# Kernel optimization log

Hardware: AMD Instinct MI355X
Metric: run time of the kernel (lower is better)

Reference implementation:

```python
import jax, jax.numpy as jnp
import numpy as np

B, C, H, W = 16, 512, 32, 32
HEADS = 8
GROUPS = 32
EPS = 1e-5


def setup_inputs() -> dict:
    key = jax.random.key(0)
    ks = jax.random.split(key, 6)
    x = jax.random.normal(ks[0], (B, C, H, W), dtype=jnp.float32)
    gn_scale = jnp.ones((C,), dtype=jnp.float32)
    gn_bias = jnp.zeros((C,), dtype=jnp.float32)
    # 1x1 convs stored as dense matrices [out, in]
    qkv_w = jax.random.normal(ks[1], (3 * C, C), dtype=jnp.float32) * (1.0 / np.sqrt(C))
    proj_w = jax.random.normal(ks[2], (C, C), dtype=jnp.float32) * (1.0 / np.sqrt(C))
    proj_b = jax.random.normal(ks[3], (C,), dtype=jnp.float32) * 0.01
    return {"x": x, "gn_scale": gn_scale, "gn_bias": gn_bias,
            "qkv_w": qkv_w, "proj_w": proj_w, "proj_b": proj_b}


def _forward(x, gn_scale, gn_bias, qkv_w, proj_w, proj_b):
    b, c, h, w = x.shape
    d = c // HEADS  # head dim
    n = h * w
    # GroupNorm over (channels_per_group, h, w)
    xg = x.reshape(b, GROUPS, c // GROUPS, h, w)
    mu = jnp.mean(xg, axis=(2, 3, 4), keepdims=True)
    var = jnp.var(xg, axis=(2, 3, 4), keepdims=True)
    xn = ((xg - mu) * jax.lax.rsqrt(var + EPS)).reshape(b, c, h, w)
    xn = xn * gn_scale[None, :, None, None] + gn_bias[None, :, None, None]
    # 1x1 conv QKV: [b, 3c, n]
    qkv = jnp.einsum('oc,bcn->bon', qkv_w, xn.reshape(b, c, n))
    # split order: (qkv, heads, d)
    qkv = qkv.reshape(b, 3, HEADS, d, n)
    q, k, v = qkv[:, 0], qkv[:, 1], qkv[:, 2]  # each [b, heads, d, n]
    k = jax.nn.softmax(k, axis=-1)
    att = jnp.einsum('bhdn,bhen->bhde', k, v)          # [b, heads, d, d]
    out = jnp.einsum('bhde,bhdn->bhen', att, q)        # [b, heads, d, n]
    out = out.reshape(b, c, h, w)
    # 1x1 proj conv with bias
    out = jnp.einsum('oc,bchw->bohw', proj_w, out) + proj_b[None, :, None, None]
    return out


def reference(x, gn_scale, gn_bias, qkv_w, proj_w, proj_b):
    return _forward(x, gn_scale, gn_bias, qkv_w, proj_w, proj_b)
```

## Files before the change

### kernel.cpp

```cpp
#include <hip/hip_runtime.h>
#include <cstdint>
#include <cstddef>

#define B_ 16
#define C_ 512
#define N_ 1024
#define HEADS_ 8
#define D_ 64
#define CPG_ 16

typedef __bf16 bf16;
typedef bf16 bf16x4 __attribute__((ext_vector_type(4)));
typedef bf16 bf16x8 __attribute__((ext_vector_type(8)));
typedef bf16 bf16x16 __attribute__((ext_vector_type(16)));
typedef float f32x4 __attribute__((ext_vector_type(4)));

__device__ __forceinline__ void gload16(void* lds, const void* g) {
    __builtin_amdgcn_global_load_lds(
        (__attribute__((address_space(1))) void*)(void*)g,
        (__attribute__((address_space(3))) void*)lds, 16, 0, 0);
}

__global__ __launch_bounds__(256) void f32_to_bf16_k(const float* __restrict__ s,
                                                     bf16* __restrict__ d, int n) {
    int i = (blockIdx.x * 256 + threadIdx.x) * 4;
    if (i < n) {
        f32x4 v = *(const f32x4*)(s + i);
        bf16x4 o = {(bf16)v[0], (bf16)v[1], (bf16)v[2], (bf16)v[3]};
        *(bf16x4*)(d + i) = o;
    }
}

__global__ __launch_bounds__(256) void gn_kernel(const float* __restrict__ x,
                                                 const float* __restrict__ gamma,
                                                 const float* __restrict__ beta,
                                                 bf16* __restrict__ xnT) {
    const int blk = blockIdx.x;
    const int b = blk >> 5, g = blk & 31;
    const int c0 = g * CPG_;
    const float* xb = x + ((size_t)b * C_ + c0) * N_;
    const int t = threadIdx.x;

    f32x4 vals[CPG_];
    float sum = 0.f, ssq = 0.f;
#pragma unroll
    for (int c = 0; c < CPG_; ++c) {
        f32x4 v = *(const f32x4*)(xb + c * N_ + t * 4);
        vals[c] = v;
#pragma unroll
        for (int j = 0; j < 4; ++j) { sum += v[j]; ssq += v[j] * v[j]; }
    }
#pragma unroll
    for (int off = 32; off >= 1; off >>= 1) {
        sum += __shfl_xor(sum, off);
        ssq += __shfl_xor(ssq, off);
    }
    __shared__ float red[2][4];
    const int wv = t >> 6, lane = t & 63;
    if (lane == 0) { red[0][wv] = sum; red[1][wv] = ssq; }
    __syncthreads();
    sum = red[0][0] + red[0][1] + red[0][2] + red[0][3];
    ssq = red[1][0] + red[1][1] + red[1][2] + red[1][3];
    const float inv = 1.f / (float)(CPG_ * N_);
    float mean = sum * inv;
    float var = ssq * inv - mean * mean;
    float rstd = rsqrtf(var + 1e-5f);
    float ga[CPG_], be[CPG_];
#pragma unroll
    for (int c = 0; c < CPG_; ++c) {
        float gm = gamma[c0 + c] * rstd;
        ga[c] = gm;
        be[c] = beta[c0 + c] - mean * gm;
    }
#pragma unroll
    for (int j = 0; j < 4; ++j) {
        int n = t * 4 + j;
        bf16x16 o;
#pragma unroll
        for (int c = 0; c < CPG_; ++c) o[c] = (bf16)(vals[c][j] * ga[c] + be[c]);
        *(bf16x16*)(xnT + ((size_t)b * N_ + n) * C_ + c0) = o;
    }
}

template <int EPI>
__global__ __launch_bounds__(256, 2) void gemm_bt(const bf16* __restrict__ A,
                                                  const bf16* __restrict__ Bt,
                                                  int M, int N, int K,
                                                  void* __restrict__ o0,
                                                  void* __restrict__ o1,
                                                  void* __restrict__ o2,
                                                  const float* __restrict__ bias) {
    __shared__ __align__(16) bf16 As[2][128][64];
    __shared__ __align__(16) bf16 Bs[2][128][64];
    const int t = threadIdx.x;
    const int lane = t & 63, wv = t >> 6;
    const int wr = wv >> 1, wc = wv & 1;
    const int bn = blockIdx.x, bm = blockIdx.y, b = blockIdx.z;
    const bf16* Ab = A + (size_t)bm * 128 * K;
    const bf16* Bb = Bt + ((size_t)b * N + (size_t)bn * 128) * K;

    f32x4 acc[4][4];
#pragma unroll
    for (int mi = 0; mi < 4; ++mi)
#pragma unroll
        for (int ni = 0; ni < 4; ++ni) acc[mi][ni] = f32x4{0.f, 0.f, 0.f, 0.f};

    const int nk = K >> 6;

    auto stage = [&](int buf, int kt) {
#pragma unroll
        for (int rnd = 0; rnd < 4; ++rnd) {
            int idx = rnd * 256 + t;
            int row = idx >> 3, pb = idx & 7;
            int srcb = pb ^ (row & 7);
            gload16((char*)&As[buf][0][0] + (size_t)idx * 16,
                    Ab + (size_t)row * K + kt * 64 + srcb * 8);
        }
#pragma unroll
        for (int rnd = 0; rnd < 4; ++rnd) {
            int idx = rnd * 256 + t;
            int row = idx >> 3, pb = idx & 7;
            int srcb = pb ^ (row & 7);
            gload16((char*)&Bs[buf][0][0] + (size_t)idx * 16,
                    Bb + (size_t)row * K + kt * 64 + srcb * 8);
        }
    };
    auto compute = [&](int buf) {
#pragma unroll
        for (int ks = 0; ks < 2; ++ks) {
            bf16x8 af[4], bfr[4];
#pragma unroll
            for (int mi = 0; mi < 4; ++mi) {
                int r = wr * 64 + mi * 16 + (lane & 15);
                int bi = (ks * 4 + (lane >> 4)) ^ (r & 7);
                af[mi] = *(const bf16x8*)&As[buf][r][bi * 8];
            }
#pragma unroll
            for (int ni = 0; ni < 4; ++ni) {
                int r = wc * 64 + ni * 16 + (lane & 15);
                int bi = (ks * 4 + (lane >> 4)) ^ (r & 7);
                bfr[ni] = *(const bf16x8*)&Bs[buf][r][bi * 8];
            }
#pragma unroll
            for (int mi = 0; mi < 4; ++mi)
#pragma unroll
                for (int ni = 0; ni < 4; ++ni)
                    acc[mi][ni] = __builtin_amdgcn_mfma_f32_16x16x32_bf16(
                        af[mi], bfr[ni], acc[mi][ni], 0, 0, 0);
        }
    };

    stage(0, 0);
    for (int kt = 0; kt < nk; ++kt) {
        const int cur = kt & 1;
        if (kt + 1 < nk) {
            stage(cur ^ 1, kt + 1);
            asm volatile("s_waitcnt vmcnt(8)" ::: "memory");
        } else {
            asm volatile("s_waitcnt vmcnt(0)" ::: "memory");
        }
        __builtin_amdgcn_s_barrier();
        __builtin_amdgcn_sched_barrier(0);
        compute(cur);
        __builtin_amdgcn_s_barrier();
    }

    const int rowb = bm * 128 + wr * 64;
    const int colb = bn * 128 + wc * 64;
#pragma unroll
    for (int mi = 0; mi < 4; ++mi) {
#pragma unroll
        for (int ni = 0; ni < 4; ++ni) {
            int r0 = rowb + mi * 16 + (lane >> 4) * 4;
            int cc = colb + ni * 16 + (lane & 15);
            if constexpr (EPI == 0) {
                bf16* qT = (bf16*)o0;
                bf16* klog = (bf16*)o1;
                bf16* vb = (bf16*)o2;
                if (r0 < 512) {
                    int h = r0 >> 6, d = r0 & 63;
                    bf16x4 pk;
#pragma unroll
                    for (int j = 0; j < 4; ++j) pk[j] = (bf16)acc[mi][ni][j];
                    *(bf16x4*)(qT + (((size_t)b * HEADS_ + h) * N_ + cc) * D_ + d) = pk;
                } else {
                    bf16* dst = (r0 < 1024) ? klog : vb;
                    int h = (r0 >> 6) & 7, d = r0 & 63;
                    bf16* p = dst + (((size_t)b * HEADS_ + h) * D_ + d) * N_ + cc;
#pragma unroll
                    for (int j = 0; j < 4; ++j) p[(size_t)j * N_] = (bf16)acc[mi][ni][j];
                }
            } else {
                float* outp = (float*)o0;
#pragma unroll
                for (int j = 0; j < 4; ++j)
                    outp[((size_t)b * C_ + r0 + j) * N_ + cc] = acc[mi][ni][j] + bias[r0 + j];
            }
        }
    }
}

__global__ __launch_bounds__(256) void softmax_k(const bf16* __restrict__ klog,
                                                 bf16* __restrict__ ksm) {
    const int row = blockIdx.x * 4 + (threadIdx.x >> 6);
    const int lane = threadIdx.x & 63;
    const bf16* rp = klog + (size_t)row * N_;
    float v[16];
    float mx = -1e30f;
#pragma unroll
    for (int i = 0; i < 2; ++i) {
        bf16x8 u = *(const bf16x8*)(rp + ((size_t)lane + 64 * i) * 8);
#pragma unroll
        for (int j = 0; j < 8; ++j) {
            v[i * 8 + j] = (float)u[j];
            mx = fmaxf(mx, v[i * 8 + j]);
        }
    }
#pragma unroll
    for (int off = 32; off >= 1; off >>= 1) mx = fmaxf(mx, __shfl_xor(mx, off));
    float s = 0.f;
#pragma unroll
    for (int i = 0; i < 16; ++i) { v[i] = __expf(v[i] - mx); s += v[i]; }
#pragma unroll
    for (int off = 32; off >= 1; off >>= 1) s += __shfl_xor(s, off);
    float inv = 1.f / s;
    bf16* op = ksm + (size_t)row * N_;
#pragma unroll
    for (int i = 0; i < 2; ++i) {
        bf16x8 o;
#pragma unroll
        for (int j = 0; j < 8; ++j) o[j] = (bf16)(v[i * 8 + j] * inv);
        *(bf16x8*)(op + ((size_t)lane + 64 * i) * 8) = o;
    }
}

__global__ __launch_bounds__(256) void attn1_kernel(const bf16* __restrict__ ksm,
                                                    const bf16* __restrict__ vb,
                                                    float* __restrict__ attP) {
    __shared__ float attp[2][64][64];
    const int blk = blockIdx.x;
    const int bh = blk >> 1, half = blk & 1;
    const int t = threadIdx.x, lane = t & 63, wv = t >> 6;
    const bf16* kb = ksm + (size_t)bh * D_ * N_;
    const bf16* vv = vb + (size_t)bh * D_ * N_;

    f32x4 acc[4][4];
#pragma unroll
    for (int mi = 0; mi < 4; ++mi)
#pragma unroll
        for (int ni = 0; ni < 4; ++ni) acc[mi][ni] = f32x4{0.f, 0.f, 0.f, 0.f};

    const int k0 = half * 512 + wv * 128;
#pragma unroll
    for (int kk = 0; kk < 128; kk += 32) {
        bf16x8 af[4], bfr[4];
#pragma unroll
        for (int mi = 0; mi < 4; ++mi)
            af[mi] = *(const bf16x8*)(kb + (size_t)(mi * 16 + (lane & 15)) * N_ + k0 + kk + (lane >> 4) * 8);
#pragma unroll
        for (int ni = 0; ni < 4; ++ni)
            bfr[ni] = *(const bf16x8*)(vv + (size_t)(ni * 16 + (lane & 15)) * N_ + k0 + kk + (lane >> 4) * 8);
#pragma unroll
        for (int mi = 0; mi < 4; ++mi)
#pragma unroll
            for (int ni = 0; ni < 4; ++ni)
                acc[mi][ni] = __builtin_amdgcn_mfma_f32_16x16x32_bf16(
                    af[mi], bfr[ni], acc[mi][ni], 0, 0, 0);
    }
    if (wv < 2) {
#pragma unroll
        for (int mi = 0; mi < 4; ++mi)
#pragma unroll
            for (int ni = 0; ni < 4; ++ni)
#pragma unroll
                for (int j = 0; j < 4; ++j)
                    attp[wv][mi * 16 + (lane >> 4) * 4 + j][ni * 16 + (lane & 15)] = acc[mi][ni][j];
    }
    __syncthreads();
    if (wv >= 2) {
#pragma unroll
        for (int mi = 0; mi < 4; ++mi)
#pragma unroll
            for (int ni = 0; ni < 4; ++ni)
#pragma unroll
                for (int j = 0; j < 4; ++j)
                    attp[wv - 2][mi * 16 + (lane >> 4) * 4 + j][ni * 16 + (lane & 15)] += acc[mi][ni][j];
    }
    __syncthreads();
    float* op = attP + (size_t)blk * 4096;
    for (int i = t; i < 4096; i += 256) {
        int d = i >> 6, e = i & 63;
        op[i] = attp[0][d][e] + attp[1][d][e];
    }
}

__global__ __launch_bounds__(256) void attn2_kernel(const float* __restrict__ attP,
                                                    const bf16* __restrict__ qT,
                                                    bf16* __restrict__ o2T) {
    __shared__ __align__(16) bf16 attT[64][64];
    const int blk = blockIdx.x;
    const int bh = blk >> 2, nc = blk & 3;
    const int b = bh >> 3, h = bh & 7;
    const int t = threadIdx.x, lane = t & 63, wv = t >> 6;
    const float* p0 = attP + (size_t)(bh * 2) * 4096;
    const float* p1 = p0 + 4096;
    for (int i = t; i < 4096; i += 256) {
        int d = i >> 6, e = i & 63;
        attT[e][d ^ ((e & 7) << 3)] = (bf16)(p0[i] + p1[i]);
    }
    __syncthreads();

    const bf16* qb = qT + (size_t)bh * N_ * D_;
    const int n0 = nc * 256 + wv * 64;
    f32x4 a2[4][4];
#pragma unroll
    for (int mi = 0; mi < 4; ++mi)
#pragma unroll
        for (int ni = 0; ni < 4; ++ni) a2[mi][ni] = f32x4{0.f, 0.f, 0.f, 0.f};
#pragma unroll
    for (int ks = 0; ks < 2; ++ks) {
        bf16x8 af[4], bfr[4];
#pragma unroll
        for (int mi = 0; mi < 4; ++mi) {
            int r = mi * 16 + (lane & 15);
            int cb = ks * 32 + (lane >> 4) * 8;
            af[mi] = *(const bf16x8*)&attT[r][cb ^ ((r & 7) << 3)];
        }
#pragma unroll
        for (int ni = 0; ni < 4; ++ni)
            bfr[ni] = *(const bf16x8*)(qb + (size_t)(n0 + ni * 16 + (lane & 15)) * D_ + ks * 32 + (lane >> 4) * 8);
#pragma unroll
        for (int mi = 0; mi < 4; ++mi)
#pragma unroll
            for (int ni = 0; ni < 4; ++ni)
                a2[mi][ni] = __builtin_amdgcn_mfma_f32_16x16x32_bf16(
                    af[mi], bfr[ni], a2[mi][ni], 0, 0, 0);
    }
#pragma unroll
    for (int mi = 0; mi < 4; ++mi) {
#pragma unroll
        for (int ni = 0; ni < 4; ++ni) {
            int e0 = mi * 16 + (lane >> 4) * 4;
            int nn = n0 + ni * 16 + (lane & 15);
            bf16x4 pk;
#pragma unroll
            for (int j = 0; j < 4; ++j) pk[j] = (bf16)a2[mi][ni][j];
            *(bf16x4*)(o2T + ((size_t)b * N_ + nn) * C_ + h * D_ + e0) = pk;
        }
    }
}

extern "C" void kernel_launch(void* const* d_in, const int* in_sizes, int n_in,
                              void* d_out, int out_size, void* d_ws, size_t ws_size,
                              hipStream_t stream) {
    const float* x = (const float*)d_in[0];
    const float* gn_scale = (const float*)d_in[1];
    const float* gn_bias = (const float*)d_in[2];
    const float* qkv_w = (const float*)d_in[3];
    const float* proj_w = (const float*)d_in[4];
    const float* proj_b = (const float*)d_in[5];
    float* out = (float*)d_out;

    const size_t elems = (size_t)B_ * C_ * N_;
    const size_t plane = (size_t)B_ * HEADS_ * D_ * N_;
    char* w = (char*)d_ws;
    bf16* xnT = (bf16*)w;   w += elems * 2;
    bf16* qT = (bf16*)w;    w += plane * 2;
    bf16* klog = (bf16*)w;  w += plane * 2;
    bf16* ksm = (bf16*)w;   w += plane * 2;
    bf16* vbuf = (bf16*)w;  w += plane * 2;
    float* attP = (float*)w; w += (size_t)256 * 4096 * 4;
    bf16* wqkv = (bf16*)w;  w += (size_t)3 * C_ * C_ * 2;
    bf16* wproj = (bf16*)w; w += (size_t)C_ * C_ * 2;
    bf16* o2T = xnT;

    f32_to_bf16_k<<<768, 256, 0, stream>>>(qkv_w, wqkv, 3 * C_ * C_);
    f32_to_bf16_k<<<256, 256, 0, stream>>>(proj_w, wproj, C_ * C_);
    gn_kernel<<<512, 256, 0, stream>>>(x, gn_scale, gn_bias, xnT);
    gemm_bt<0><<<dim3(8, 12, 16), 256, 0, stream>>>(wqkv, xnT, 1536, 1024, 512,
                                                    (void*)qT, (void*)klog, (void*)vbuf, nullptr);
    softmax_k<<<2048, 256, 0, stream>>>(klog, ksm);
    attn1_kernel<<<256, 256, 0, stream>>>(ksm, vbuf, attP);
    attn2_kernel<<<512, 256, 0, stream>>>(attP, qT, o2T);
    gemm_bt<1><<<dim3(8, 4, 16), 256, 0, stream>>>(wproj, o2T, 512, 1024, 512,
                                                   (void*)out, nullptr, nullptr, proj_b);
}
```

Before: 181.6 us.

## Fuse softmax normalization into attn1 via row stats; merge weight conversions

The softmax kernel now writes only per-row max and reciprocal sum instead of a full normalized K tensor. attn1 reads the raw K logits and applies exp and scale on the fly while loading operands. This removes one bf16 plane write and read, about 16 MB. The two weight-conversion launches are merged into one, and the templated GEMM is split into two specialized kernels with compile-time K. In exchange, attn1 does more exp work in its inner loop.

```diff
diff --git a/kernel.cpp b/kernel.cpp
--- a/kernel.cpp
+++ b/kernel.cpp
@@ -8,6 +8,7 @@
 #define HEADS_ 8
 #define D_ 64
 #define CPG_ 16
+#define KDIM 512
 
 typedef __bf16 bf16;
 typedef bf16 bf16x4 __attribute__((ext_vector_type(4)));
@@ -21,14 +22,19 @@
         (__attribute__((address_space(3))) void*)lds, 16, 0, 0);
 }
 
-__global__ __launch_bounds__(256) void f32_to_bf16_k(const float* __restrict__ s,
-                                                     bf16* __restrict__ d, int n) {
-    int i = (blockIdx.x * 256 + threadIdx.x) * 4;
-    if (i < n) {
-        f32x4 v = *(const f32x4*)(s + i);
-        bf16x4 o = {(bf16)v[0], (bf16)v[1], (bf16)v[2], (bf16)v[3]};
-        *(bf16x4*)(d + i) = o;
-    }
+__global__ __launch_bounds__(256) void convert_w(const float* __restrict__ qkv_w,
+                                                 const float* __restrict__ proj_w,
+                                                 bf16* __restrict__ wqkv,
+                                                 bf16* __restrict__ wproj) {
+    const int bid = blockIdx.x;
+    const float* s;
+    bf16* d;
+    int i;
+    if (bid < 768) { s = qkv_w; d = wqkv; i = bid * 1024 + threadIdx.x * 4; }
+    else           { s = proj_w; d = wproj; i = (bid - 768) * 1024 + threadIdx.x * 4; }
+    f32x4 v = *(const f32x4*)(s + i);
+    bf16x4 o = {(bf16)v[0], (bf16)v[1], (bf16)v[2], (bf16)v[3]};
+    *(bf16x4*)(d + i) = o;
 }
 
 __global__ __launch_bounds__(256) void gn_kernel(const float* __restrict__ x,
@@ -82,22 +88,19 @@
     }
 }
 
-template <int EPI>
-__global__ __launch_bounds__(256, 2) void gemm_bt(const bf16* __restrict__ A,
-                                                  const bf16* __restrict__ Bt,
-                                                  int M, int N, int K,
-                                                  void* __restrict__ o0,
-                                                  void* __restrict__ o1,
-                                                  void* __restrict__ o2,
-                                                  const float* __restrict__ bias) {
+__global__ __launch_bounds__(256, 2) void qkv_gemm(const bf16* __restrict__ A,
+                                                   const bf16* __restrict__ Bt,
+                                                   bf16* __restrict__ qT,
+                                                   bf16* __restrict__ klog,
+                                                   bf16* __restrict__ vb) {
     __shared__ __align__(16) bf16 As[2][128][64];
     __shared__ __align__(16) bf16 Bs[2][128][64];
     const int t = threadIdx.x;
     const int lane = t & 63, wv = t >> 6;
     const int wr = wv >> 1, wc = wv & 1;
     const int bn = blockIdx.x, bm = blockIdx.y, b = blockIdx.z;
-    const bf16* Ab = A + (size_t)bm * 128 * K;
-    const bf16* Bb = Bt + ((size_t)b * N + (size_t)bn * 128) * K;
+    const bf16* Ab = A + (size_t)bm * 128 * KDIM;
+    const bf16* Bb = Bt + ((size_t)b * N_ + (size_t)bn * 128) * KDIM;
 
     f32x4 acc[4][4];
 #pragma unroll
@@ -105,7 +108,7 @@
 #pragma unroll
         for (int ni = 0; ni < 4; ++ni) acc[mi][ni] = f32x4{0.f, 0.f, 0.f, 0.f};
 
-    const int nk = K >> 6;
+    const int nk = KDIM >> 6;
 
     auto stage = [&](int buf, int kt) {
 #pragma unroll
@@ -114,7 +117,7 @@
             int row = idx >> 3, pb = idx & 7;
             int srcb = pb ^ (row & 7);
             gload16((char*)&As[buf][0][0] + (size_t)idx * 16,
-                    Ab + (size_t)row * K + kt * 64 + srcb * 8);
+                    Ab + (size_t)row * KDIM + kt * 64 + srcb * 8);
         }
 #pragma unroll
         for (int rnd = 0; rnd < 4; ++rnd) {
@@ -122,7 +125,7 @@
             int row = idx >> 3, pb = idx & 7;
             int srcb = pb ^ (row & 7);
             gload16((char*)&Bs[buf][0][0] + (size_t)idx * 16,
-                    Bb + (size_t)row * K + kt * 64 + srcb * 8);
+                    Bb + (size_t)row * KDIM + kt * 64 + srcb * 8);
         }
     };
     auto compute = [&](int buf) {
@@ -173,35 +176,119 @@
         for (int ni = 0; ni < 4; ++ni) {
             int r0 = rowb + mi * 16 + (lane >> 4) * 4;
             int cc = colb + ni * 16 + (lane & 15);
-            if constexpr (EPI == 0) {
-                bf16* qT = (bf16*)o0;
-                bf16* klog = (bf16*)o1;
-                bf16* vb = (bf16*)o2;
-                if (r0 < 512) {
-                    int h = r0 >> 6, d = r0 & 63;
-                    bf16x4 pk;
-#pragma unroll
-                    for (int j = 0; j < 4; ++j) pk[j] = (bf16)acc[mi][ni][j];
-                    *(bf16x4*)(qT + (((size_t)b * HEADS_ + h) * N_ + cc) * D_ + d) = pk;
-                } else {
-                    bf16* dst = (r0 < 1024) ? klog : vb;
-                    int h = (r0 >> 6) & 7, d = r0 & 63;
-                    bf16* p = dst + (((size_t)b * HEADS_ + h) * D_ + d) * N_ + cc;
-#pragma unroll
-                    for (int j = 0; j < 4; ++j) p[(size_t)j * N_] = (bf16)acc[mi][ni][j];
-                }
+            if (r0 < 512) {
+                int h = r0 >> 6, d = r0 & 63;
+                bf16x4 pk;
+#pragma unroll
+                for (int j = 0; j < 4; ++j) pk[j] = (bf16)acc[mi][ni][j];
+                *(bf16x4*)(qT + (((size_t)b * HEADS_ + h) * N_ + cc) * D_ + d) = pk;
             } else {
-                float* outp = (float*)o0;
-#pragma unroll
-                for (int j = 0; j < 4; ++j)
-                    outp[((size_t)b * C_ + r0 + j) * N_ + cc] = acc[mi][ni][j] + bias[r0 + j];
+                bf16* dst = (r0 < 1024) ? klog : vb;
+                int h = (r0 >> 6) & 7, d = r0 & 63;
+                bf16* p = dst + (((size_t)b * HEADS_ + h) * D_ + d) * N_ + cc;
+#pragma unroll
+                for (int j = 0; j < 4; ++j) p[(size_t)j * N_] = (bf16)acc[mi][ni][j];
             }
         }
     }
 }
 
-__global__ __launch_bounds__(256) void softmax_k(const bf16* __restrict__ klog,
-                                                 bf16* __restrict__ ksm) {
+__global__ __launch_bounds__(256, 2) void proj_gemm(const bf16* __restrict__ A,
+                                                    const bf16* __restrict__ Bt,
+                                                    float* __restrict__ outp,
+                                                    const float* __restrict__ bias) {
+    __shared__ __align__(16) bf16 As[2][128][64];
+    __shared__ __align__(16) bf16 Bs[2][128][64];
+    const int t = threadIdx.x;
+    const int lane = t & 63, wv = t >> 6;
+    const int wr = wv >> 1, wc = wv & 1;
+    const int bn = blockIdx.x, bm = blockIdx.y, b = blockIdx.z;
+    const bf16* Ab = A + (size_t)bm * 128 * KDIM;
+    const bf16* Bb = Bt + ((size_t)b * N_ + (size_t)bn * 128) * KDIM;
+
+    f32x4 acc[4][4];
+#pragma unroll
+    for (int mi = 0; mi < 4; ++mi)
+#pragma unroll
+        for (int ni = 0; ni < 4; ++ni) acc[mi][ni] = f32x4{0.f, 0.f, 0.f, 0.f};
+
+    const int nk = KDIM >> 6;
+
+    auto stage = [&](int buf, int kt) {
+#pragma unroll
+        for (int rnd = 0; rnd < 4; ++rnd) {
+            int idx = rnd * 256 + t;
+            int row = idx >> 3, pb = idx & 7;
+            int srcb = pb ^ (row & 7);
+            gload16((char*)&As[buf][0][0] + (size_t)idx * 16,
+                    Ab + (size_t)row * KDIM + kt * 64 + srcb * 8);
+        }
+#pragma unroll
+        for (int rnd = 0; rnd < 4; ++rnd) {
+            int idx = rnd * 256 + t;
+            int row = idx >> 3, pb = idx & 7;
+            int srcb = pb ^ (row & 7);
+            gload16((char*)&Bs[buf][0][0] + (size_t)idx * 16,
+                    Bb + (size_t)row * KDIM + kt * 64 + srcb * 8);
+        }
+    };
+    auto compute = [&](int buf) {
+#pragma unroll
+        for (int ks = 0; ks < 2; ++ks) {
+            bf16x8 af[4], bfr[4];
+#pragma unroll
+            for (int mi = 0; mi < 4; ++mi) {
+                int r = wr * 64 + mi * 16 + (lane & 15);
+                int bi = (ks * 4 + (lane >> 4)) ^ (r & 7);
+                af[mi] = *(const bf16x8*)&As[buf][r][bi * 8];
+            }
+#pragma unroll
+            for (int ni = 0; ni < 4; ++ni) {
+                int r = wc * 64 + ni * 16 + (lane & 15);
+                int bi = (ks * 4 + (lane >> 4)) ^ (r & 7);
+                bfr[ni] = *(const bf16x8*)&Bs[buf][r][bi * 8];
+            }
+#pragma unroll
+            for (int mi = 0; mi < 4; ++mi)
+#pragma unroll
+                for (int ni = 0; ni < 4; ++ni)
+                    acc[mi][ni] = __builtin_amdgcn_mfma_f32_16x16x32_bf16(
+                        af[mi], bfr[ni], acc[mi][ni], 0, 0, 0);
+        }
+    };
+
+    stage(0, 0);
+    for (int kt = 0; kt < nk; ++kt) {
+        const int cur = kt & 1;
+        if (kt + 1 < nk) {
+            stage(cur ^ 1, kt + 1);
+            asm volatile("s_waitcnt vmcnt(8)" ::: "memory");
+        } else {
+            asm volatile("s_waitcnt vmcnt(0)" ::: "memory");
+        }
+        __builtin_amdgcn_s_barrier();
+        __builtin_amdgcn_sched_barrier(0);
+        compute(cur);
+        __builtin_amdgcn_s_barrier();
+    }
+
+    const int rowb = bm * 128 + wr * 64;
+    const int colb = bn * 128 + wc * 64;
+#pragma unroll
+    for (int mi = 0; mi < 4; ++mi) {
+#pragma unroll
+        for (int ni = 0; ni < 4; ++ni) {
+            int r0 = rowb + mi * 16 + (lane >> 4) * 4;
+            int cc = colb + ni * 16 + (lane & 15);
+#pragma unroll
+            for (int j = 0; j < 4; ++j)
+                outp[((size_t)b * C_ + r0 + j) * N_ + cc] = acc[mi][ni][j] + bias[r0 + j];
+        }
+    }
+}
+
+__global__ __launch_bounds__(256) void kstats_k(const bf16* __restrict__ klog,
+                                                float2* __restrict__ kstat) {
     const int row = blockIdx.x * 4 + (threadIdx.x >> 6);
     const int lane = threadIdx.x & 63;
     const bf16* rp = klog + (size_t)row * N_;
@@ -220,29 +307,27 @@
     for (int off = 32; off >= 1; off >>= 1) mx = fmaxf(mx, __shfl_xor(mx, off));
     float s = 0.f;
 #pragma unroll
-    for (int i = 0; i < 16; ++i) { v[i] = __expf(v[i] - mx); s += v[i]; }
+    for (int i = 0; i < 16; ++i) s += __expf(v[i] - mx);
 #pragma unroll
     for (int off = 32; off >= 1; off >>= 1) s += __shfl_xor(s, off);
-    float inv = 1.f / s;
-    bf16* op = ksm + (size_t)row * N_;
-#pragma unroll
-    for (int i = 0; i < 2; ++i) {
-        bf16x8 o;
-#pragma unroll
-        for (int j = 0; j < 8; ++j) o[j] = (bf16)(v[i * 8 + j] * inv);
-        *(bf16x8*)(op + ((size_t)lane + 64 * i) * 8) = o;
-    }
-}
-
-__global__ __launch_bounds__(256) void attn1_kernel(const bf16* __restrict__ ksm,
+    if (lane == 0) kstat[row] = make_float2(mx, 1.f / s);
+}
+
+__global__ __launch_bounds__(256) void attn1_kernel(const bf16* __restrict__ klog,
+                                                    const float2* __restrict__ kstat,
                                                     const bf16* __restrict__ vb,
                                                     float* __restrict__ attP) {
     __shared__ float attp[2][64][64];
     const int blk = blockIdx.x;
     const int bh = blk >> 1, half = blk & 1;
     const int t = threadIdx.x, lane = t & 63, wv = t >> 6;
-    const bf16* kb = ksm + (size_t)bh * D_ * N_;
+    const bf16* kb = klog + (size_t)bh * D_ * N_;
     const bf16* vv = vb + (size_t)bh * D_ * N_;
+
+    float2 kst[4];
+#pragma unroll
+    for (int mi = 0; mi < 4; ++mi)
+        kst[mi] = kstat[(size_t)bh * D_ + mi * 16 + (lane & 15)];
 
     f32x4 acc[4][4];
 #pragma unroll
@@ -255,8 +340,14 @@
     for (int kk = 0; kk < 128; kk += 32) {
         bf16x8 af[4], bfr[4];
 #pragma unroll
-        for (int mi = 0; mi < 4; ++mi)
-            af[mi] = *(const bf16x8*)(kb + (size_t)(mi * 16 + (lane & 15)) * N_ + k0 + kk + (lane >> 4) * 8);
+        for (int mi = 0; mi < 4; ++mi) {
+            bf16x8 raw = *(const bf16x8*)(kb + (size_t)(mi * 16 + (lane & 15)) * N_ + k0 + kk + (lane >> 4) * 8);
+            bf16x8 a;
+#pragma unroll
+            for (int j = 0; j < 8; ++j)
+                a[j] = (bf16)(__expf((float)raw[j] - kst[mi].x) * kst[mi].y);
+            af[mi] = a;
+        }
 #pragma unroll
         for (int ni = 0; ni < 4; ++ni)
             bfr[ni] = *(const bf16x8*)(vv + (size_t)(ni * 16 + (lane & 15)) * N_ + k0 + kk + (lane >> 4) * 8);
@@ -364,24 +455,21 @@
     const size_t elems = (size_t)B_ * C_ * N_;
     const size_t plane = (size_t)B_ * HEADS_ * D_ * N_;
     char* w = (char*)d_ws;
-    bf16* xnT = (bf16*)w;   w += elems * 2;
-    bf16* qT = (bf16*)w;    w += plane * 2;
-    bf16* klog = (bf16*)w;  w += plane * 2;
-    bf16* ksm = (bf16*)w;   w += plane * 2;
-    bf16* vbuf = (bf16*)w;  w += plane * 2;
+    bf16* xnT = (bf16*)w;    w += elems * 2;
+    bf16* qT = (bf16*)w;     w += plane * 2;
+    bf16* klog = (bf16*)w;   w += plane * 2;
+    bf16* vbuf = (bf16*)w;   w += plane * 2;
     float* attP = (float*)w; w += (size_t)256 * 4096 * 4;
-    bf16* wqkv = (bf16*)w;  w += (size_t)3 * C_ * C_ * 2;
-    bf16* wproj = (bf16*)w; w += (size_t)C_ * C_ * 2;
+    float2* kstat = (float2*)w; w += (size_t)8192 * 8;
+    bf16* wqkv = (bf16*)w;   w += (size_t)3 * C_ * C_ * 2;
+    bf16* wproj = (bf16*)w;  w += (size_t)C_ * C_ * 2;
     bf16* o2T = xnT;
 
-    f32_to_bf16_k<<<768, 256, 0, stream>>>(qkv_w, wqkv, 3 * C_ * C_);
-    f32_to_bf16_k<<<256, 256, 0, stream>>>(proj_w, wproj, C_ * C_);
+    convert_w<<<1024, 256, 0, stream>>>(qkv_w, proj_w, wqkv, wproj);
     gn_kernel<<<512, 256, 0, stream>>>(x, gn_scale, gn_bias, xnT);
-    gemm_bt<0><<<dim3(8, 12, 16), 256, 0, stream>>>(wqkv, xnT, 1536, 1024, 512,
-                                                    (void*)qT, (void*)klog, (void*)vbuf, nullptr);
-    softmax_k<<<2048, 256, 0, stream>>>(klog, ksm);
-    attn1_kernel<<<256, 256, 0, stream>>>(ksm, vbuf, attP);
+    qkv_gemm<<<dim3(8, 12, 16), 256, 0, stream>>>(wqkv, xnT, qT, klog, vbuf);
+    kstats_k<<<2048, 256, 0, stream>>>(klog, kstat);
+    attn1_kernel<<<256, 256, 0, stream>>>(klog, kstat, vbuf, attP);
     attn2_kernel<<<512, 256, 0, stream>>>(attP, qT, o2T);
-    gemm_bt<1><<<dim3(8, 4, 16), 256, 0, stream>>>(wproj, o2T, 512, 1024, 512,
-                                                   (void*)out, nullptr, nullptr, proj_b);
-}
+    proj_gemm<<<dim3(8, 4, 16), 256, 0, stream>>>(wproj, o2T, out, proj_b);
+}
```

Result: faster. 172.3 us (-5.1%).
